# Performance work log

Measured on AMD Instinct MI355X. Metric: run time of the kernel, lower is better.

## Reference

```python
import jax, jax.numpy as jnp
import numpy as np

H_DIM = 64      # input_dim of edge_aggregation (== h_dim)
HID = 128       # hidden_size of each per-edge-type agg MLP
T = 5           # edge_types for non-nba dataset
B, E, N = 64, 1024, 512


def setup_inputs() -> dict:
    key = jax.random.key(0)
    ks = jax.random.split(key, 8)
    edge_distribution = jax.random.uniform(ks[0], (B, E, T), dtype=jnp.float32)
    H = jax.random.uniform(ks[1], (B, E, N), dtype=jnp.float32)
    ori = jax.random.normal(ks[2], (B, N, H_DIM), dtype=jnp.float32)
    s1 = 1.0 / np.sqrt(H_DIM)
    s2 = 1.0 / np.sqrt(HID)
    # stacked per-edge-type MLP params: Linear(64->128) -> ReLU -> Linear(128->64)
    W1 = jax.random.uniform(ks[3], (T, H_DIM, HID), minval=-s1, maxval=s1, dtype=jnp.float32)
    b1 = jax.random.uniform(ks[4], (T, HID), minval=-s1, maxval=s1, dtype=jnp.float32)
    W2 = jax.random.uniform(ks[5], (T, HID, H_DIM), minval=-s2, maxval=s2, dtype=jnp.float32)
    b2 = jax.random.uniform(ks[6], (T, H_DIM), minval=-s2, maxval=s2, dtype=jnp.float32)
    return {"edge_distribution": edge_distribution, "H": H, "ori": ori,
            "W1": W1, "b1": b1, "W2": W2, "b2": b2}


def reference(edge_distribution, H, ori, W1, b1, W2, b2):
    # incidence gather: hyperedge features [B, E, D]
    edges = jnp.matmul(H, ori)
    # per-edge-type 2-layer MLP, vectorized over the T edge types
    h = jax.nn.relu(jnp.einsum('bed,tdh->bteh', edges, W1) + b1[None, :, None, :])
    per_type = jnp.einsum('bteh,thd->bted', h, W2) + b2[None, :, None, :]
    # mixture-weighted sum over edge types -> [B, E, D]
    edge_feature = jnp.einsum('bet,bted->bed', edge_distribution, per_type)
    # scatter back through H^T and concat with original node features
    node_agg = jnp.einsum('ben,bed->bnd', H, edge_feature)  # H^T @ edge_feature
    node_feature = jnp.concatenate((node_agg, ori), axis=-1)  # [B, N, 2D]
    return node_feature
```

## Files before the change

kernel.cpp:

```cpp
#include <hip/hip_runtime.h>

#define B_   64
#define E_   1024
#define N_   512
#define D_   64
#define HID_ 128
#define T_   5

typedef __bf16 bf16x8 __attribute__((ext_vector_type(8)));
typedef float f32x4 __attribute__((ext_vector_type(4)));

__device__ __forceinline__ unsigned short f2bu(float f) {
    union { float f; unsigned int u; } v; v.f = f;
    unsigned int r = (v.u + 0x7fffu + ((v.u >> 16) & 1u)) >> 16;
    return (unsigned short)r;
}

__device__ __forceinline__ unsigned int pack2(float lo, float hi) {
    union { __bf16 b[2]; unsigned int u; } v;
    v.b[0] = (__bf16)lo; v.b[1] = (__bf16)hi;
    return v.u;
}

__device__ __forceinline__ uint4 cvt8(float4 a, float4 b) {
    union { __bf16 h[8]; uint4 u; } v;
    v.h[0] = (__bf16)a.x; v.h[1] = (__bf16)a.y; v.h[2] = (__bf16)a.z; v.h[3] = (__bf16)a.w;
    v.h[4] = (__bf16)b.x; v.h[5] = (__bf16)b.y; v.h[6] = (__bf16)b.z; v.h[7] = (__bf16)b.w;
    return v.u;
}

#define MFMA16(a, b, c) __builtin_amdgcn_mfma_f32_16x16x32_bf16((a), (b), (c), 0, 0, 0)

#define RBAR() do {                                          \
    __builtin_amdgcn_sched_barrier(0);                       \
    asm volatile("s_waitcnt lgkmcnt(0)" ::: "memory");       \
    __builtin_amdgcn_s_barrier();                            \
    __builtin_amdgcn_sched_barrier(0);                       \
} while (0)

__global__ __launch_bounds__(256) void k_prep_w(const float* __restrict__ W1,
                                                const float* __restrict__ W2,
                                                unsigned short* __restrict__ W1T,
                                                unsigned short* __restrict__ W2T) {
    int idx = blockIdx.x * 256 + threadIdx.x;
    if (idx < T_ * HID_ * D_) {
        int t = idx / (HID_ * D_), rem = idx % (HID_ * D_);
        int h = rem / D_, d = rem % D_;
        W1T[idx] = f2bu(W1[(t * D_ + d) * HID_ + h]);
    } else {
        int j = idx - T_ * HID_ * D_;
        int t = j / (D_ * HID_), rem = j % (D_ * HID_);
        int d = rem / HID_, h = rem % HID_;
        W2T[j] = f2bu(W2[(t * HID_ + h) * D_ + d]);
    }
}

__global__ __launch_bounds__(256) void k_ori_prep(const float* __restrict__ ori,
                                                  float* __restrict__ out,
                                                  unsigned short* __restrict__ oriT) {
    int b = blockIdx.y, n0 = blockIdx.x * 64;
    __shared__ float tl[64 * 65];
    int tid = threadIdx.x;
    int dl = tid & 63;
    #pragma unroll 4
    for (int p = 0; p < 16; ++p) {
        int nn = p * 4 + (tid >> 6);
        float v = ori[(size_t)(b * N_ + n0 + nn) * D_ + dl];
        out[(size_t)(b * N_ + n0 + nn) * 128 + 64 + dl] = v;
        tl[dl * 65 + nn] = v;
    }
    __syncthreads();
    #pragma unroll 4
    for (int p = 0; p < 16; ++p) {
        int dd = p * 4 + (tid >> 6);
        oriT[(size_t)(b * D_ + dd) * N_ + n0 + dl] = f2bu(tl[dd * 65 + dl]);
    }
}

__global__ __launch_bounds__(256, 2) void k_edge_mlp(const float* __restrict__ H,
                                                     const unsigned short* __restrict__ oriT,
                                                     const float* __restrict__ ed,
                                                     const float* __restrict__ b1,
                                                     const float* __restrict__ b2,
                                                     const unsigned short* __restrict__ W1T,
                                                     const unsigned short* __restrict__ W2T,
                                                     unsigned short* __restrict__ efT) {
    int bx = blockIdx.x;
    int b = bx >> 4, e0 = (bx & 15) * 64;
    __shared__ __align__(16) unsigned short X[16384];
    __shared__ __align__(16) unsigned short a_sh[64 * 64];
    __shared__ __align__(16) unsigned short h_sh[64 * 128];
    __shared__ float wd_sh[320];
    __shared__ float b1_sh[640];
    __shared__ float b2_sh[320];
    int tid = threadIdx.x, w = tid >> 6, l = tid & 63, q = l >> 4, c = l & 15;
    int rs = tid >> 3, sgs = tid & 7;
    int swsl = (sgs ^ (rs & 7)) * 8;

    for (int u = tid; u < 320; u += 256) wd_sh[u] = ed[((size_t)b * E_ + e0) * T_ + u];
    for (int u = tid; u < 640; u += 256) b1_sh[u] = b1[u];
    for (int u = tid; u < 320; u += 256) b2_sh[u] = b2[u];

    const f32x4 zero = {0.f, 0.f, 0.f, 0.f};

    f32x4 acc1[4];
    #pragma unroll
    for (int fn = 0; fn < 4; ++fn) acc1[fn] = zero;

    const float* Hb = &H[((size_t)b * E_ + e0) * N_];
    const unsigned short* Ob = &oriT[(size_t)b * D_ * N_];

    float4 f00, f01, f10, f11;
    uint4 ob0, ob1;
    uint4 wr1[4], wr2[4];

    {
        const float* s0 = Hb + (size_t)rs * N_ + sgs * 8;
        const float* s1 = Hb + (size_t)(rs + 32) * N_ + sgs * 8;
        f00 = *(const float4*)&s0[0]; f01 = *(const float4*)&s0[4];
        f10 = *(const float4*)&s1[0]; f11 = *(const float4*)&s1[4];
        ob0 = *(const uint4*)&Ob[(size_t)rs * N_ + sgs * 8];
        ob1 = *(const uint4*)&Ob[(size_t)(rs + 32) * N_ + sgs * 8];
    }
    {
        unsigned short* aA = X;
        unsigned short* bB = X + 4096;
        *(uint4*)&aA[rs * 64 + swsl] = cvt8(f00, f01);
        *(uint4*)&aA[(rs + 32) * 64 + swsl] = cvt8(f10, f11);
        *(uint4*)&bB[rs * 64 + swsl] = ob0;
        *(uint4*)&bB[(rs + 32) * 64 + swsl] = ob1;
    }
    RBAR();

    #pragma unroll
    for (int ks = 0; ks < 8; ++ks) {
        if (ks < 7) {
            int k0 = (ks + 1) * 64;
            const float* s0 = Hb + (size_t)rs * N_ + k0 + sgs * 8;
            const float* s1 = Hb + (size_t)(rs + 32) * N_ + k0 + sgs * 8;
            f00 = *(const float4*)&s0[0]; f01 = *(const float4*)&s0[4];
            f10 = *(const float4*)&s1[0]; f11 = *(const float4*)&s1[4];
            ob0 = *(const uint4*)&Ob[(size_t)rs * N_ + k0 + sgs * 8];
            ob1 = *(const uint4*)&Ob[(size_t)(rs + 32) * N_ + k0 + sgs * 8];
        }
        if (ks == 7) {
            #pragma unroll
            for (int p = 0; p < 4; ++p) {
                int u2 = p * 256 + tid;
                wr1[p] = *(const uint4*)&W1T[(size_t)(u2 >> 3) * D_ + (u2 & 7) * 8];
                wr2[p] = *(const uint4*)&W2T[(size_t)(u2 >> 4) * HID_ + (u2 & 15) * 8];
            }
        }
        const unsigned short* aA = X + (ks & 1) * 8192;
        const unsigned short* bB = aA + 4096;
        #pragma unroll
        for (int hh = 0; hh < 2; ++hh) {
            int sl = ((hh * 4 + q) ^ (c & 7)) * 8;
            bf16x8 a0 = *(const bf16x8*)&aA[(w * 16 + c) * 64 + sl];
            #pragma unroll
            for (int fn = 0; fn < 4; ++fn) {
                bf16x8 bb = *(const bf16x8*)&bB[(fn * 16 + c) * 64 + sl];
                acc1[fn] = MFMA16(a0, bb, acc1[fn]);
            }
        }
        if (ks < 7) {
            unsigned short* aN = X + ((ks & 1) ^ 1) * 8192;
            unsigned short* bN = aN + 4096;
            *(uint4*)&aN[rs * 64 + swsl] = cvt8(f00, f01);
            *(uint4*)&aN[(rs + 32) * 64 + swsl] = cvt8(f10, f11);
            *(uint4*)&bN[rs * 64 + swsl] = ob0;
            *(uint4*)&bN[(rs + 32) * 64 + swsl] = ob1;
            RBAR();
        }
    }

    #pragma unroll
    for (int fn = 0; fn < 4; ++fn)
        #pragma unroll
        for (int i = 0; i < 4; ++i) {
            int row = w * 16 + q * 4 + i;
            a_sh[row * 64 + ((fn * 16 + c) ^ ((row & 7) << 3))] = f2bu(acc1[fn][i]);
        }
    bf16x8 afr[2];
    #pragma unroll
    for (int ks2 = 0; ks2 < 2; ++ks2)
        afr[ks2] = *(const bf16x8*)&a_sh[(w * 16 + c) * 64 + (((ks2 * 4 + q) ^ (c & 7)) * 8)];

    RBAR();

    unsigned short* w1_sh = X;
    unsigned short* w2_sh = X + 8192;

    f32x4 y[4];
    #pragma unroll
    for (int fn = 0; fn < 4; ++fn) y[fn] = zero;

    #pragma unroll
    for (int t = 0; t < T_; ++t) {
        #pragma unroll
        for (int p = 0; p < 4; ++p) {
            int u2 = p * 256 + tid, hh = u2 >> 3, sg = u2 & 7;
            *(uint4*)&w1_sh[hh * 64 + ((sg ^ (hh & 7)) * 8)] = wr1[p];
        }
        #pragma unroll
        for (int p = 0; p < 4; ++p) {
            int u2 = p * 256 + tid, dd = u2 >> 4, sg = u2 & 15;
            *(uint4*)&w2_sh[dd * 128 + ((sg ^ (dd & 7)) * 8)] = wr2[p];
        }
        RBAR();
        if (t < T_ - 1) {
            #pragma unroll
            for (int p = 0; p < 4; ++p) {
                int u2 = p * 256 + tid;
                wr1[p] = *(const uint4*)&W1T[((size_t)(t + 1) * HID_ + (u2 >> 3)) * D_ + (u2 & 7) * 8];
                wr2[p] = *(const uint4*)&W2T[((size_t)(t + 1) * D_ + (u2 >> 4)) * HID_ + (u2 & 15) * 8];
            }
        }
        f32x4 hc[8];
        #pragma unroll
        for (int fn = 0; fn < 8; ++fn) hc[fn] = zero;
        #pragma unroll
        for (int ks2 = 0; ks2 < 2; ++ks2) {
            #pragma unroll
            for (int fn = 0; fn < 8; ++fn) {
                bf16x8 bb = *(const bf16x8*)&w1_sh[(fn * 16 + c) * 64 + (((ks2 * 4 + q) ^ (c & 7)) * 8)];
                hc[fn] = MFMA16(afr[ks2], bb, hc[fn]);
            }
        }
        float wv[4];
        #pragma unroll
        for (int i = 0; i < 4; ++i) wv[i] = wd_sh[(w * 16 + q * 4 + i) * T_ + t];
        #pragma unroll
        for (int fn = 0; fn < 8; ++fn) {
            float b1v = b1_sh[t * HID_ + fn * 16 + c];
            #pragma unroll
            for (int i = 0; i < 4; ++i) {
                float v = hc[fn][i] + b1v;
                v = fmaxf(v, 0.0f) * wv[i];
                int row = q * 4 + i;
                h_sh[(w * 16 + row) * 128 + ((fn * 16 + c) ^ ((row & 7) << 3))] = f2bu(v);
            }
        }
        #pragma unroll
        for (int ks2 = 0; ks2 < 4; ++ks2) {
            bf16x8 a = *(const bf16x8*)&h_sh[(w * 16 + c) * 128 + (((ks2 * 4 + q) ^ (c & 7)) * 8)];
            #pragma unroll
            for (int fn = 0; fn < 4; ++fn) {
                bf16x8 bb = *(const bf16x8*)&w2_sh[(fn * 16 + c) * 128 + (((ks2 * 4 + q) ^ (c & 7)) * 8)];
                y[fn] = MFMA16(a, bb, y[fn]);
            }
        }
        RBAR();
    }

    #pragma unroll
    for (int fn = 0; fn < 4; ++fn) {
        int d = fn * 16 + c;
        ushort4 o;
        #pragma unroll
        for (int i = 0; i < 4; ++i) {
            int r = w * 16 + q * 4 + i;
            float s = y[fn][i];
            #pragma unroll
            for (int t = 0; t < T_; ++t) s += wd_sh[r * T_ + t] * b2_sh[t * D_ + d];
            ((unsigned short*)&o)[i] = f2bu(s);
        }
        *(ushort4*)&efT[((size_t)b * D_ + d) * E_ + e0 + w * 16 + q * 4] = o;
    }
}

__global__ __launch_bounds__(256) void k_gemm_out(const float* __restrict__ H,
                                                  const unsigned short* __restrict__ efT,
                                                  float* __restrict__ out) {
    int bid = blockIdx.x;
    int swz = (bid & 7) * 64 + (bid >> 3);
    int b = swz >> 3, n0 = (swz & 7) * 64;
    __shared__ __align__(16) unsigned short aA[2][64 * 72];
    __shared__ unsigned int bB32[2][64 * 33];
    int tid = threadIdx.x, w = tid >> 6, l = tid & 63, q = l >> 4, c = l & 15;
    int r2 = tid >> 3, cg = tid & 7;
    const f32x4 zero = {0.f, 0.f, 0.f, 0.f};
    f32x4 acc[4];
    #pragma unroll
    for (int fm = 0; fm < 4; ++fm) acc[fm] = zero;

    const unsigned short* Ab = &efT[(size_t)b * D_ * E_];
    const float* Hb = &H[(size_t)b * E_ * N_ + n0];

    uint4 ar0, ar1;
    float4 f0, f1, g0, g1;
    {
        ar0 = *(const uint4*)&Ab[(size_t)r2 * E_ + cg * 8];
        ar1 = *(const uint4*)&Ab[(size_t)(r2 + 32) * E_ + cg * 8];
        const float* s0 = Hb + (size_t)(2 * r2) * N_ + cg * 8;
        const float* s1 = s0 + N_;
        f0 = *(const float4*)&s0[0]; f1 = *(const float4*)&s0[4];
        g0 = *(const float4*)&s1[0]; g1 = *(const float4*)&s1[4];
    }
    {
        *(uint4*)&aA[0][r2 * 72 + cg * 8] = ar0;
        *(uint4*)&aA[0][(r2 + 32) * 72 + cg * 8] = ar1;
        float r0a[8] = {f0.x, f0.y, f0.z, f0.w, f1.x, f1.y, f1.z, f1.w};
        float r1a[8] = {g0.x, g0.y, g0.z, g0.w, g1.x, g1.y, g1.z, g1.w};
        #pragma unroll
        for (int j = 0; j < 8; ++j)
            bB32[0][(cg * 8 + j) * 33 + r2] = pack2(r0a[j], r1a[j]);
    }
    __syncthreads();

    for (int ks = 0; ks < 16; ++ks) {
        if (ks < 15) {
            int k0 = (ks + 1) * 64;
            ar0 = *(const uint4*)&Ab[(size_t)r2 * E_ + k0 + cg * 8];
            ar1 = *(const uint4*)&Ab[(size_t)(r2 + 32) * E_ + k0 + cg * 8];
            const float* s0 = Hb + (size_t)(k0 + 2 * r2) * N_ + cg * 8;
            const float* s1 = s0 + N_;
            f0 = *(const float4*)&s0[0]; f1 = *(const float4*)&s0[4];
            g0 = *(const float4*)&s1[0]; g1 = *(const float4*)&s1[4];
        }
        int cur = ks & 1;
        #pragma unroll
        for (int hh = 0; hh < 2; ++hh) {
            union { unsigned int u[4]; bf16x8 v; } bb;
            #pragma unroll
            for (int i = 0; i < 4; ++i)
                bb.u[i] = bB32[cur][(w * 16 + c) * 33 + hh * 16 + q * 4 + i];
            #pragma unroll
            for (int fm = 0; fm < 4; ++fm) {
                bf16x8 afr = *(const bf16x8*)&aA[cur][(fm * 16 + c) * 72 + hh * 32 + q * 8];
                acc[fm] = MFMA16(afr, bb.v, acc[fm]);
            }
        }
        if (ks < 15) {
            int nxt = cur ^ 1;
            *(uint4*)&aA[nxt][r2 * 72 + cg * 8] = ar0;
            *(uint4*)&aA[nxt][(r2 + 32) * 72 + cg * 8] = ar1;
            float r0a[8] = {f0.x, f0.y, f0.z, f0.w, f1.x, f1.y, f1.z, f1.w};
            float r1a[8] = {g0.x, g0.y, g0.z, g0.w, g1.x, g1.y, g1.z, g1.w};
            #pragma unroll
            for (int j = 0; j < 8; ++j)
                bB32[nxt][(cg * 8 + j) * 33 + r2] = pack2(r0a[j], r1a[j]);
            __syncthreads();
        }
    }
    #pragma unroll
    for (int fm = 0; fm < 4; ++fm) {
        *(f32x4*)&out[((size_t)b * N_ + n0 + w * 16 + c) * 128 + fm * 16 + q * 4] = acc[fm];
    }
}

extern "C" void kernel_launch(void* const* d_in, const int* in_sizes, int n_in,
                              void* d_out, int out_size, void* d_ws, size_t ws_size,
                              hipStream_t stream) {
    const float* ed  = (const float*)d_in[0];
    const float* H   = (const float*)d_in[1];
    const float* ori = (const float*)d_in[2];
    const float* W1  = (const float*)d_in[3];
    const float* b1  = (const float*)d_in[4];
    const float* W2  = (const float*)d_in[5];
    const float* b2  = (const float*)d_in[6];
    float* out = (float*)d_out;

    char* ws = (char*)d_ws;
    size_t used = 0;
    unsigned short* oriT = (unsigned short*)(ws + used); used += (size_t)B_ * D_ * N_ * 2;
    unsigned short* W1T  = (unsigned short*)(ws + used); used += (size_t)T_ * HID_ * D_ * 2;
    unsigned short* W2T  = (unsigned short*)(ws + used); used += (size_t)T_ * D_ * HID_ * 2;
    unsigned short* efT  = (unsigned short*)(ws + used); used += (size_t)B_ * D_ * E_ * 2;

    hipLaunchKernelGGL(k_prep_w, dim3(320), dim3(256), 0, stream, W1, W2, W1T, W2T);
    hipLaunchKernelGGL(k_ori_prep, dim3(8, 64), dim3(256), 0, stream, ori, out, oriT);
    hipLaunchKernelGGL(k_edge_mlp, dim3(1024), dim3(256), 0, stream,
                       H, oriT, ed, b1, b2, W1T, W2T, efT);
    hipLaunchKernelGGL(k_gemm_out, dim3(512), dim3(256), 0, stream, H, efT, out);
}
```

Before: 266.4 us.

## Deepen H prefetch to two stages, raise edge-MLP occupancy, merge prep kernels

The edge-MLP kernel now prefetches H tiles two k-steps ahead using two register sets, so global loads of the dominant fp32 H stream have more time to land. It reuses the X staging buffer for a_sh to cut shared memory and raises the launch bound to 3 blocks per CU. The two prep kernels are merged into one launch with block-index dispatch to save a launch. The extra prefetch registers and the higher occupancy target may force spills or register pressure.

```diff
diff --git a/kernel.cpp b/kernel.cpp
--- a/kernel.cpp
+++ b/kernel.cpp
@@ -38,29 +38,31 @@
     __builtin_amdgcn_sched_barrier(0);                       \
 } while (0)
 
-__global__ __launch_bounds__(256) void k_prep_w(const float* __restrict__ W1,
-                                                const float* __restrict__ W2,
-                                                unsigned short* __restrict__ W1T,
-                                                unsigned short* __restrict__ W2T) {
-    int idx = blockIdx.x * 256 + threadIdx.x;
-    if (idx < T_ * HID_ * D_) {
-        int t = idx / (HID_ * D_), rem = idx % (HID_ * D_);
-        int h = rem / D_, d = rem % D_;
-        W1T[idx] = f2bu(W1[(t * D_ + d) * HID_ + h]);
-    } else {
-        int j = idx - T_ * HID_ * D_;
-        int t = j / (D_ * HID_), rem = j % (D_ * HID_);
-        int d = rem / HID_, h = rem % HID_;
-        W2T[j] = f2bu(W2[(t * HID_ + h) * D_ + d]);
-    }
-}
-
-__global__ __launch_bounds__(256) void k_ori_prep(const float* __restrict__ ori,
-                                                  float* __restrict__ out,
-                                                  unsigned short* __restrict__ oriT) {
-    int b = blockIdx.y, n0 = blockIdx.x * 64;
+__global__ __launch_bounds__(256) void k_prep(const float* __restrict__ W1,
+                                              const float* __restrict__ W2,
+                                              const float* __restrict__ ori,
+                                              unsigned short* __restrict__ W1T,
+                                              unsigned short* __restrict__ W2T,
+                                              float* __restrict__ out,
+                                              unsigned short* __restrict__ oriT) {
     __shared__ float tl[64 * 65];
     int tid = threadIdx.x;
+    if (blockIdx.x < 320) {
+        int idx = blockIdx.x * 256 + tid;
+        if (idx < T_ * HID_ * D_) {
+            int t = idx / (HID_ * D_), rem = idx % (HID_ * D_);
+            int h = rem / D_, d = rem % D_;
+            W1T[idx] = f2bu(W1[(t * D_ + d) * HID_ + h]);
+        } else {
+            int j = idx - T_ * HID_ * D_;
+            int t = j / (D_ * HID_), rem = j % (D_ * HID_);
+            int d = rem / HID_, h = rem % HID_;
+            W2T[j] = f2bu(W2[(t * HID_ + h) * D_ + d]);
+        }
+        return;
+    }
+    int id = blockIdx.x - 320;
+    int b = id >> 3, n0 = (id & 7) * 64;
     int dl = tid & 63;
     #pragma unroll 4
     for (int p = 0; p < 16; ++p) {
@@ -77,7 +79,7 @@
     }
 }
 
-__global__ __launch_bounds__(256, 2) void k_edge_mlp(const float* __restrict__ H,
+__global__ __launch_bounds__(256, 3) void k_edge_mlp(const float* __restrict__ H,
                                                      const unsigned short* __restrict__ oriT,
                                                      const float* __restrict__ ed,
                                                      const float* __restrict__ b1,
@@ -88,7 +90,6 @@
     int bx = blockIdx.x;
     int b = bx >> 4, e0 = (bx & 15) * 64;
     __shared__ __align__(16) unsigned short X[16384];
-    __shared__ __align__(16) unsigned short a_sh[64 * 64];
     __shared__ __align__(16) unsigned short h_sh[64 * 128];
     __shared__ float wd_sh[320];
     __shared__ float b1_sh[640];
@@ -110,39 +111,43 @@
     const float* Hb = &H[((size_t)b * E_ + e0) * N_];
     const unsigned short* Ob = &oriT[(size_t)b * D_ * N_];
 
-    float4 f00, f01, f10, f11;
-    uint4 ob0, ob1;
+    float4 hA0, hA1, hA2, hA3;
+    float4 hB0, hB1, hB2, hB3;
+    uint4 or0, or1;
     uint4 wr1[4], wr2[4];
 
-    {
-        const float* s0 = Hb + (size_t)rs * N_ + sgs * 8;
-        const float* s1 = Hb + (size_t)(rs + 32) * N_ + sgs * 8;
-        f00 = *(const float4*)&s0[0]; f01 = *(const float4*)&s0[4];
-        f10 = *(const float4*)&s1[0]; f11 = *(const float4*)&s1[4];
-        ob0 = *(const uint4*)&Ob[(size_t)rs * N_ + sgs * 8];
-        ob1 = *(const uint4*)&Ob[(size_t)(rs + 32) * N_ + sgs * 8];
-    }
-    {
-        unsigned short* aA = X;
-        unsigned short* bB = X + 4096;
-        *(uint4*)&aA[rs * 64 + swsl] = cvt8(f00, f01);
-        *(uint4*)&aA[(rs + 32) * 64 + swsl] = cvt8(f10, f11);
-        *(uint4*)&bB[rs * 64 + swsl] = ob0;
-        *(uint4*)&bB[(rs + 32) * 64 + swsl] = ob1;
-    }
+#define P1_LOADH(F0, F1, F2, F3, k0) do {                                     \
+        const float* s0_ = Hb + (size_t)rs * N_ + (k0) + sgs * 8;             \
+        const float* s1_ = Hb + (size_t)(rs + 32) * N_ + (k0) + sgs * 8;      \
+        F0 = *(const float4*)&s0_[0]; F1 = *(const float4*)&s0_[4];           \
+        F2 = *(const float4*)&s1_[0]; F3 = *(const float4*)&s1_[4];           \
+    } while (0)
+#define P1_LOADO(k0) do {                                                     \
+        or0 = *(const uint4*)&Ob[(size_t)rs * N_ + (k0) + sgs * 8];           \
+        or1 = *(const uint4*)&Ob[(size_t)(rs + 32) * N_ + (k0) + sgs * 8];    \
+    } while (0)
+#define P1_WRITE(bufi, F0, F1, F2, F3) do {                                   \
+        unsigned short* aW_ = X + (bufi) * 8192;                              \
+        unsigned short* bW_ = aW_ + 4096;                                     \
+        *(uint4*)&aW_[rs * 64 + swsl] = cvt8(F0, F1);                         \
+        *(uint4*)&aW_[(rs + 32) * 64 + swsl] = cvt8(F2, F3);                  \
+        *(uint4*)&bW_[rs * 64 + swsl] = or0;                                  \
+        *(uint4*)&bW_[(rs + 32) * 64 + swsl] = or1;                           \
+    } while (0)
+
+    P1_LOADH(hA0, hA1, hA2, hA3, 0);
+    P1_LOADH(hB0, hB1, hB2, hB3, 64);
+    P1_LOADO(0);
+    P1_WRITE(0, hA0, hA1, hA2, hA3);
     RBAR();
 
     #pragma unroll
     for (int ks = 0; ks < 8; ++ks) {
-        if (ks < 7) {
-            int k0 = (ks + 1) * 64;
-            const float* s0 = Hb + (size_t)rs * N_ + k0 + sgs * 8;
-            const float* s1 = Hb + (size_t)(rs + 32) * N_ + k0 + sgs * 8;
-            f00 = *(const float4*)&s0[0]; f01 = *(const float4*)&s0[4];
-            f10 = *(const float4*)&s1[0]; f11 = *(const float4*)&s1[4];
-            ob0 = *(const uint4*)&Ob[(size_t)rs * N_ + k0 + sgs * 8];
-            ob1 = *(const uint4*)&Ob[(size_t)(rs + 32) * N_ + k0 + sgs * 8];
-        }
+        if (ks < 6) {
+            if ((ks & 1) == 0) P1_LOADH(hA0, hA1, hA2, hA3, (ks + 2) * 64);
+            else               P1_LOADH(hB0, hB1, hB2, hB3, (ks + 2) * 64);
+        }
+        if (ks < 7) P1_LOADO((ks + 1) * 64);
         if (ks == 7) {
             #pragma unroll
             for (int p = 0; p < 4; ++p) {
@@ -164,16 +169,13 @@
             }
         }
         if (ks < 7) {
-            unsigned short* aN = X + ((ks & 1) ^ 1) * 8192;
-            unsigned short* bN = aN + 4096;
-            *(uint4*)&aN[rs * 64 + swsl] = cvt8(f00, f01);
-            *(uint4*)&aN[(rs + 32) * 64 + swsl] = cvt8(f10, f11);
-            *(uint4*)&bN[rs * 64 + swsl] = ob0;
-            *(uint4*)&bN[(rs + 32) * 64 + swsl] = ob1;
+            if (((ks + 1) & 1) == 0) P1_WRITE(0, hA0, hA1, hA2, hA3);
+            else                     P1_WRITE(1, hB0, hB1, hB2, hB3);
             RBAR();
         }
     }
 
+    unsigned short* a_sh = X;
     #pragma unroll
     for (int fn = 0; fn < 4; ++fn)
         #pragma unroll
@@ -267,6 +269,9 @@
         }
         *(ushort4*)&efT[((size_t)b * D_ + d) * E_ + e0 + w * 16 + q * 4] = o;
     }
+#undef P1_LOADH
+#undef P1_LOADO
+#undef P1_WRITE
 }
 
 __global__ __launch_bounds__(256) void k_gemm_out(const float* __restrict__ H,
@@ -368,8 +373,8 @@
     unsigned short* W2T  = (unsigned short*)(ws + used); used += (size_t)T_ * D_ * HID_ * 2;
     unsigned short* efT  = (unsigned short*)(ws + used); used += (size_t)B_ * D_ * E_ * 2;
 
-    hipLaunchKernelGGL(k_prep_w, dim3(320), dim3(256), 0, stream, W1, W2, W1T, W2T);
-    hipLaunchKernelGGL(k_ori_prep, dim3(8, 64), dim3(256), 0, stream, ori, out, oriT);
+    hipLaunchKernelGGL(k_prep, dim3(832), dim3(256), 0, stream,
+                       W1, W2, ori, W1T, W2T, out, oriT);
     hipLaunchKernelGGL(k_edge_mlp, dim3(1024), dim3(256), 0, stream,
                        H, oriT, ed, b1, b2, W1T, W2T, efT);
     hipLaunchKernelGGL(k_gemm_out, dim3(512), dim3(256), 0, stream, H, efT, out);
```

Result: no change. 268.0 us (+0.6%).
